# Optimization experiments

Measured on AMD Instinct MI355X. Metric: run time of the kernel, lower is better.

## Reference

```python
import jax, jax.numpy as jnp
import numpy as np

B, S, D = 2, 2048, 2048
NH, HD = 32, 64          # query heads, head_dim
NKV, NREP = 8, 4         # kv heads, num_key_value_groups
ROPE_THETA = 10000.0


def _rope_cos_sin(seq_len, head_dim, dtype=jnp.float32):
    inv_freq = 1.0 / (ROPE_THETA ** (jnp.arange(0, head_dim, 2, dtype=jnp.float32) / head_dim))
    pos = jnp.arange(seq_len, dtype=jnp.float32)
    freqs = jnp.outer(pos, inv_freq)               # [S, HD/2]
    emb = jnp.concatenate([freqs, freqs], axis=-1)  # [S, HD]
    return jnp.cos(emb).astype(dtype), jnp.sin(emb).astype(dtype)


def _rotate_half(x):
    x1, x2 = jnp.split(x, 2, axis=-1)
    return jnp.concatenate([-x2, x1], axis=-1)


def setup_inputs() -> dict:
    key = jax.random.key(0)
    k1, k2, k3, k4, k5 = jax.random.split(key, 5)
    scale = 0.02
    hidden_states = jax.random.normal(k1, (B, S, D), dtype=jnp.float32)
    Wq = jax.random.normal(k2, (NH * HD, D), dtype=jnp.float32) * scale
    Wk = jax.random.normal(k3, (NKV * HD, D), dtype=jnp.float32) * scale
    Wv = jax.random.normal(k4, (NKV * HD, D), dtype=jnp.float32) * scale
    Wo = jax.random.normal(k5, (D, NH * HD), dtype=jnp.float32) * scale
    # additive causal mask [B, 1, S, S]: 0 on/below diagonal, large negative above
    causal = jnp.triu(jnp.full((S, S), -1e9, dtype=jnp.float32), k=1)
    attention_mask = jnp.broadcast_to(causal[None, None], (B, 1, S, S))
    return {"hidden_states": hidden_states, "Wq": Wq, "Wk": Wk, "Wv": Wv,
            "Wo": Wo, "attention_mask": attention_mask}


def reference(hidden_states, Wq, Wk, Wv, Wo, attention_mask):
    bsz, q_len, _ = hidden_states.shape
    # projections (torch Linear: x @ W^T)
    q = (hidden_states @ Wq.T).reshape(bsz, q_len, NH, HD).transpose(0, 2, 1, 3)   # [B,NH,S,HD]
    k = (hidden_states @ Wk.T).reshape(bsz, q_len, NKV, HD).transpose(0, 2, 1, 3)  # [B,NKV,S,HD]
    v = (hidden_states @ Wv.T).reshape(bsz, q_len, NKV, HD).transpose(0, 2, 1, 3)
    # RoPE
    cos, sin = _rope_cos_sin(q_len, HD, hidden_states.dtype)  # [S,HD]
    cos = cos[None, None]  # [1,1,S,HD] (unsqueeze_dim=1 over broadcast batch)
    sin = sin[None, None]
    q = q * cos + _rotate_half(q) * sin
    k = k * cos + _rotate_half(k) * sin
    # repeat_kv (GQA): [B,NKV,S,HD] -> [B,NH,S,HD]
    k = jnp.repeat(k, NREP, axis=1)
    v = jnp.repeat(v, NREP, axis=1)
    # eager attention with materialized scores (faithful to the source)
    scores = jnp.einsum('bhqd,bhkd->bhqk', q, k) / jnp.sqrt(jnp.float32(HD))
    scores = scores + attention_mask[:, :, :, :q_len]
    probs = jax.nn.softmax(scores.astype(jnp.float32), axis=-1).astype(q.dtype)
    out = jnp.einsum('bhqk,bhkd->bhqd', probs, v)          # [B,NH,S,HD]
    out = out.transpose(0, 2, 1, 3).reshape(bsz, q_len, NH * HD)
    return out @ Wo.T
```

## Files before the change

kernel.cpp:

```cpp
#include <hip/hip_runtime.h>


#define S_LEN 2048
#define D_MODEL 2048
#define NHEAD 32
#define HEAD_DIM 64
#define NKVH 8
#define M_ROWS 4096
#define KVW (NKVH * HEAD_DIM)

typedef __attribute__((ext_vector_type(4))) float f32x4;
typedef __attribute__((ext_vector_type(8))) short bf16x8;

#define MFMA16(a, b, c) __builtin_amdgcn_mfma_f32_16x16x32_bf16((a), (b), (c), 0, 0, 0)

#define GLOAD_LDS16(g, l)                                                     \
    __builtin_amdgcn_global_load_lds(                                         \
        (const __attribute__((address_space(1))) void*)(g),                   \
        (__attribute__((address_space(3))) void*)(l), 16, 0, 0)

static __device__ __forceinline__ unsigned short f2bf(float f) {
    union { __bf16 b; unsigned short u; } v;
    v.b = (__bf16)f;
    return v.u;
}

static __device__ __forceinline__ float fexp2(float x) {
#if __has_builtin(__builtin_amdgcn_exp2f)
    return __builtin_amdgcn_exp2f(x);
#else
    return exp2f(x);
#endif
}

static __device__ __forceinline__ void xcd_swz(int& bx, int& by) {
    const int gx = gridDim.x;
    const int nwg = gx * gridDim.y;
    int lin = blockIdx.y * gx + blockIdx.x;
    lin = (lin & 7) * (nwg >> 3) + (lin >> 3);
    bx = lin % gx;
    by = lin / gx;
}

static __device__ bool detect_f32_block(const unsigned short* __restrict__ h) {
    __shared__ int dcnt;
    if (threadIdx.x == 0) dcnt = 0;
    __syncthreads();
    const unsigned short v = h[2 * (threadIdx.x & 255)];
    const int e = (v >> 7) & 0xFF;
    if (threadIdx.x < 256 && e >= 0x8D) atomicAdd(&dcnt, 1);
    __syncthreads();
    return dcnt >= 8;
}

static __device__ __forceinline__ bf16x8 load_frag(bool f32p, const void* p, size_t off) {
    if (f32p) {
        const float* fp = (const float*)p + off;
        f32x4 x = *reinterpret_cast<const f32x4*>(fp);
        f32x4 y = *reinterpret_cast<const f32x4*>(fp + 4);
        bf16x8 r;
        r[0] = (short)f2bf(x[0]); r[1] = (short)f2bf(x[1]);
        r[2] = (short)f2bf(x[2]); r[3] = (short)f2bf(x[3]);
        r[4] = (short)f2bf(y[0]); r[5] = (short)f2bf(y[1]);
        r[6] = (short)f2bf(y[2]); r[7] = (short)f2bf(y[3]);
        return r;
    }
    return *reinterpret_cast<const bf16x8*>((const unsigned short*)p + off);
}

__global__ __launch_bounds__(256) void cvt_all(const void* __restrict__ h,
                                               const void* __restrict__ wq,
                                               const void* __restrict__ wk,
                                               const void* __restrict__ wv,
                                               const void* __restrict__ wo,
                                               unsigned short* __restrict__ hbuf,
                                               unsigned short* __restrict__ wqb,
                                               unsigned short* __restrict__ wkvb,
                                               unsigned short* __restrict__ wob,
                                               float2* __restrict__ ropetab) {
    const bool f32p = detect_f32_block((const unsigned short*)h);
    const int e0 = 1048576;
    const int e1 = e0 + 524288;
    const int e2 = e1 + 131072;
    const int e3 = e2 + 131072;
    const int e4 = e3 + 524288;
    const int e5 = e4 + 8192;
    int i = blockIdx.x * 256 + threadIdx.x;
    const int stride = gridDim.x * 256;
    for (; i < e5; i += stride) {
        if (i >= e4) {
            const int base = (i - e4) * 8;
#pragma unroll
            for (int j = 0; j < 8; ++j) {
                const int idx = base + j;
                const int s = idx >> 5, dd = idx & 31;
                const float inv = exp2f(-(float)dd * 0.4152410118609203f);
                const float th = (float)s * inv;
                float sn, cs;
                sincosf(th, &sn, &cs);
                ropetab[idx] = make_float2(cs, sn);
            }
            continue;
        }
        const void* s;
        unsigned short* d;
        size_t off;
        if (i < e0)      { s = h;  d = hbuf; off = (size_t)i; }
        else if (i < e1) { s = wq; d = wqb;  off = (size_t)(i - e0); }
        else if (i < e2) { s = wk; d = wkvb; off = (size_t)(i - e1); }
        else if (i < e3) { s = wv; d = wkvb + (size_t)512 * 2048; off = (size_t)(i - e2); }
        else             { s = wo; d = wob;  off = (size_t)(i - e3); }
        bf16x8 v = load_frag(f32p, s, off * 8);
        *reinterpret_cast<bf16x8*>(d + off * 8) = v;
    }
}

static __device__ __forceinline__ void rope4_tab(const float2* __restrict__ tab,
                                                 const float (&vals)[4], float (&outv)[4],
                                                 int m, int l16) {
    const int s = m & (S_LEN - 1);
#pragma unroll
    for (int nt = 0; nt < 4; ++nt) {
        const int d = nt * 16 + l16;
        const float2 cs = tab[s * 32 + (d & 31)];
        const float part = vals[nt ^ 2];
        const float rot = (nt < 2) ? -part : part;
        outv[nt] = vals[nt] * cs.x + rot * cs.y;
    }
}

static __device__ __forceinline__ void rope4(const float (&vals)[4], float (&outv)[4],
                                             int m, int l16) {
    const float sf = (float)(m & (S_LEN - 1));
#pragma unroll
    for (int nt = 0; nt < 4; ++nt) {
        const int d = nt * 16 + l16;
        const float inv = exp2f(-(float)(d & 31) * 0.4152410118609203f);
        const float th = sf * inv;
        float sn, cs;
        sincosf(th, &sn, &cs);
        const float part = vals[nt ^ 2];
        const float rot = (nt < 2) ? -part : part;
        outv[nt] = vals[nt] * cs + rot * sn;
    }
}

__global__ __launch_bounds__(256) void gemm_qkv_lds(const unsigned short* __restrict__ A,
                                                    const unsigned short* __restrict__ W,
                                                    unsigned short* __restrict__ Qo,
                                                    unsigned short* __restrict__ KVo,
                                                    const float2* __restrict__ ropetab) {
    __shared__ unsigned short lds_a[128 * 32];
    __shared__ unsigned short lds_b[128 * 32];

    const int wave = threadIdx.x >> 6;
    const int lane = threadIdx.x & 63;
    const int l16  = lane & 15;
    const int quad = lane >> 4;
    const int wm   = wave >> 1;
    const int wn   = wave & 1;

    int bx, by;
    xcd_swz(bx, by);
    const int m0 = bx * 128;
    const int n0 = by * 128;

    const int srow = lane >> 2;
    const int scol = (lane & 3) * 8;
    const unsigned short* ag[2];
    const unsigned short* wg[2];
#pragma unroll
    for (int i = 0; i < 2; ++i) {
        const int c = wave * 2 + i;
        ag[i] = A + (size_t)(m0 + c * 16 + srow) * D_MODEL + scol;
        wg[i] = W + (size_t)(n0 + c * 16 + srow) * D_MODEL + scol;
    }

    f32x4 acc[4][4];
#pragma unroll
    for (int i = 0; i < 4; ++i)
#pragma unroll
        for (int j = 0; j < 4; ++j) acc[i][j] = (f32x4){0.f, 0.f, 0.f, 0.f};

    for (int k0 = 0; k0 < D_MODEL; k0 += 32) {
#pragma unroll
        for (int i = 0; i < 2; ++i) {
            const int c = wave * 2 + i;
            GLOAD_LDS16(ag[i] + k0, &lds_a[c * 512]);
            GLOAD_LDS16(wg[i] + k0, &lds_b[c * 512]);
        }
        __syncthreads();

        bf16x8 af[4], bfm[4];
#pragma unroll
        for (int t = 0; t < 4; ++t) {
            af[t]  = *reinterpret_cast<const bf16x8*>(&lds_a[(wm * 64 + t * 16 + l16) * 32 + quad * 8]);
            bfm[t] = *reinterpret_cast<const bf16x8*>(&lds_b[(wn * 64 + t * 16 + l16) * 32 + quad * 8]);
        }
#pragma unroll
        for (int mt = 0; mt < 4; ++mt)
#pragma unroll
            for (int nt = 0; nt < 4; ++nt)
                acc[mt][nt] = MFMA16(af[mt], bfm[nt], acc[mt][nt]);
        __syncthreads();
    }

    const int ncol0 = n0 + wn * 64;
    const bool do_rope = (ncol0 < 2048 + KVW);
    unsigned short* dst;
    int cstride, c0;
    if (ncol0 < 2048) { dst = Qo;  cstride = 2048; c0 = ncol0; }
    else              { dst = KVo; cstride = 1024; c0 = ncol0 - 2048; }

#pragma unroll
    for (int mt = 0; mt < 4; ++mt) {
#pragma unroll
        for (int r = 0; r < 4; ++r) {
            const int m = m0 + wm * 64 + mt * 16 + quad * 4 + r;
            float vals[4];
#pragma unroll
            for (int nt = 0; nt < 4; ++nt) vals[nt] = acc[mt][nt][r];
            float outv[4];
            if (do_rope) {
                rope4_tab(ropetab, vals, outv, m, l16);
            } else {
#pragma unroll
                for (int nt = 0; nt < 4; ++nt) outv[nt] = vals[nt];
            }
            unsigned short* cp = dst + (size_t)m * cstride + c0;
#pragma unroll
            for (int nt = 0; nt < 4; ++nt) cp[nt * 16 + l16] = f2bf(outv[nt]);
        }
    }
}

__global__ __launch_bounds__(256) void gemm_bt_lds(const unsigned short* __restrict__ A,
                                                   const unsigned short* __restrict__ W,
                                                   void* __restrict__ Cp, int N,
                                                   const unsigned short* __restrict__ hdet,
                                                   int rope, int finalout) {
    __shared__ unsigned short lds_a[128 * 32];
    __shared__ unsigned short lds_b[128 * 32];

    bool of32 = false;
    if (finalout) of32 = detect_f32_block(hdet);

    const int wave = threadIdx.x >> 6;
    const int lane = threadIdx.x & 63;
    const int l16  = lane & 15;
    const int quad = lane >> 4;
    const int wm   = wave >> 1;
    const int wn   = wave & 1;

    int bx, by;
    xcd_swz(bx, by);
    const int m0 = bx * 128;
    const int n0 = by * 128;

    const int srow = lane >> 2;
    const int scol = (lane & 3) * 8;
    const unsigned short* ag[2];
    const unsigned short* wg[2];
#pragma unroll
    for (int i = 0; i < 2; ++i) {
        const int c = wave * 2 + i;
        ag[i] = A + (size_t)(m0 + c * 16 + srow) * D_MODEL + scol;
        wg[i] = W + (size_t)(n0 + c * 16 + srow) * D_MODEL + scol;
    }

    f32x4 acc[4][4];
#pragma unroll
    for (int i = 0; i < 4; ++i)
#pragma unroll
        for (int j = 0; j < 4; ++j) acc[i][j] = (f32x4){0.f, 0.f, 0.f, 0.f};

    for (int k0 = 0; k0 < D_MODEL; k0 += 32) {
#pragma unroll
        for (int i = 0; i < 2; ++i) {
            const int c = wave * 2 + i;
            GLOAD_LDS16(ag[i] + k0, &lds_a[c * 512]);
            GLOAD_LDS16(wg[i] + k0, &lds_b[c * 512]);
        }
        __syncthreads();

        bf16x8 af[4], bfm[4];
#pragma unroll
        for (int t = 0; t < 4; ++t) {
            af[t]  = *reinterpret_cast<const bf16x8*>(&lds_a[(wm * 64 + t * 16 + l16) * 32 + quad * 8]);
            bfm[t] = *reinterpret_cast<const bf16x8*>(&lds_b[(wn * 64 + t * 16 + l16) * 32 + quad * 8]);
        }
#pragma unroll
        for (int mt = 0; mt < 4; ++mt)
#pragma unroll
            for (int nt = 0; nt < 4; ++nt)
                acc[mt][nt] = MFMA16(af[mt], bfm[nt], acc[mt][nt]);
        __syncthreads();
    }

    const bool do_rope = (rope != 0);
    const int ncol0 = n0 + wn * 64;

#pragma unroll
    for (int mt = 0; mt < 4; ++mt) {
#pragma unroll
        for (int r = 0; r < 4; ++r) {
            const int m = m0 + wm * 64 + mt * 16 + quad * 4 + r;
            float vals[4];
#pragma unroll
            for (int nt = 0; nt < 4; ++nt) vals[nt] = acc[mt][nt][r];
            float outv[4];
            if (do_rope) {
                rope4(vals, outv, m, l16);
            } else {
#pragma unroll
                for (int nt = 0; nt < 4; ++nt) outv[nt] = vals[nt];
            }
            const size_t crow = (size_t)m * N + ncol0;
            if (of32) {
                float* cp = (float*)Cp + crow;
#pragma unroll
                for (int nt = 0; nt < 4; ++nt) cp[nt * 16 + l16] = outv[nt];
            } else {
                unsigned short* cp = (unsigned short*)Cp + crow;
#pragma unroll
                for (int nt = 0; nt < 4; ++nt) cp[nt * 16 + l16] = f2bf(outv[nt]);
            }
        }
    }
}

__global__ __launch_bounds__(256) void transpose_v(const unsigned short* __restrict__ Vsrc,
                                                   unsigned short* __restrict__ Vt) {
    __shared__ unsigned short t[64][72];
    const int bid = blockIdx.x;
    const int ct = bid & 7;
    const int st = (bid >> 3) & 31;
    const int b  = bid >> 8;
    const unsigned short* src = Vsrc + ((size_t)b * S_LEN + st * 64) * 1024 + ct * 64;
    unsigned short* dst = Vt + ((size_t)b * KVW + ct * 64) * S_LEN + st * 64;
    const int r0 = threadIdx.x >> 3;
    const int c0 = (threadIdx.x & 7) * 8;
#pragma unroll
    for (int h = 0; h < 2; ++h) {
        bf16x8 v = *reinterpret_cast<const bf16x8*>(src + (size_t)(r0 + h * 32) * 1024 + c0);
        *reinterpret_cast<bf16x8*>(&t[r0 + h * 32][c0]) = v;
    }
    __syncthreads();
#pragma unroll
    for (int h = 0; h < 2; ++h) {
        const int cr = r0 + h * 32;
        bf16x8 v;
#pragma unroll
        for (int j = 0; j < 8; ++j) v[j] = (short)t[c0 + j][cr];
        *reinterpret_cast<bf16x8*>(dst + (size_t)cr * S_LEN + c0) = v;
    }
}

struct AttnCtx {
    const unsigned short* qbase;
    const unsigned short* kbase;
    const unsigned short* vtbase;
    unsigned short* obase;
    int kvs;
    int l16, quad;
    unsigned short (*lpw)[72];
};

#define SM_C 0.18033688011112042f
#define SM_THR 8.0f

static __device__ __forceinline__ void attn_qtile(const AttnCtx& cx, int q0w) {
    const int l16 = cx.l16, quad = cx.quad;
    const int kvs = cx.kvs;

    bf16x8 ones;
#pragma unroll
    for (int j = 0; j < 8; ++j) ones[j] = (short)0x3F80;

    bf16x8 aq[2][2];
#pragma unroll
    for (int m = 0; m < 2; ++m)
#pragma unroll
        for (int kh = 0; kh < 2; ++kh)
            aq[m][kh] = *reinterpret_cast<const bf16x8*>(
                cx.qbase + (size_t)(q0w + m * 16 + l16) * D_MODEL + kh * 32 + quad * 8);

    f32x4 o[2][4];
    f32x4 c_l[2];
#pragma unroll
    for (int m = 0; m < 2; ++m) {
#pragma unroll
        for (int i = 0; i < 4; ++i) o[m][i] = (f32x4){0.f, 0.f, 0.f, 0.f};
        c_l[m] = (f32x4){0.f, 0.f, 0.f, 0.f};
    }
    float m2[2][4];
#pragma unroll
    for (int m = 0; m < 2; ++m)
#pragma unroll
        for (int r = 0; r < 4; ++r) m2[m][r] = 0.f;

    const int kv_hi = q0w + 32;

    for (int k0 = 0; k0 < kv_hi; k0 += 64) {
        bf16x8 kf[8];
#pragma unroll
        for (int t = 0; t < 4; ++t) {
            const unsigned short* krow = cx.kbase + (size_t)(k0 + t * 16 + l16) * kvs;
            kf[2 * t]     = *reinterpret_cast<const bf16x8*>(krow + quad * 8);
            kf[2 * t + 1] = *reinterpret_cast<const bf16x8*>(krow + 32 + quad * 8);
        }

        f32x4 sc[2][4];
        __builtin_amdgcn_s_setprio(1);
#pragma unroll
        for (int t = 0; t < 4; ++t) {
#pragma unroll
            for (int m = 0; m < 2; ++m) {
                f32x4 c = (f32x4){0.f, 0.f, 0.f, 0.f};
                c = MFMA16(aq[m][0], kf[2 * t], c);
                c = MFMA16(aq[m][1], kf[2 * t + 1], c);
                sc[m][t] = c;
            }
        }
        __builtin_amdgcn_s_setprio(0);

        bf16x8 vf[8];
#pragma unroll
        for (int nt = 0; nt < 4; ++nt) {
            const unsigned short* vrow =
                cx.vtbase + (size_t)(nt * 16 + l16) * S_LEN + k0 + quad * 8;
            vf[2 * nt]     = *reinterpret_cast<const bf16x8*>(vrow);
            vf[2 * nt + 1] = *reinterpret_cast<const bf16x8*>(vrow + 32);
        }

        const bool full = (k0 + 63 <= q0w);
        float pm[2][4];
        float dif = -3.0e38f;
#pragma unroll
        for (int m = 0; m < 2; ++m) {
#pragma unroll
            for (int r = 0; r < 4; ++r) {
                const int qi = q0w + m * 16 + quad * 4 + r;
                float s[4];
#pragma unroll
                for (int t = 0; t < 4; ++t) {
                    s[t] = sc[m][t][r] * SM_C;
                    if (!full && (k0 + t * 16 + l16 > qi)) s[t] = -1.0e30f;
                    sc[m][t][r] = s[t];
                }
                const float p = fmaxf(fmaxf(s[0], s[1]), fmaxf(s[2], s[3]));
                pm[m][r] = p;
                dif = fmaxf(dif, p - m2[m][r]);
            }
        }
        if (__any(dif > SM_THR)) {
#pragma unroll
            for (int m = 0; m < 2; ++m) {
#pragma unroll
                for (int r = 0; r < 4; ++r) {
                    float mt = pm[m][r];
#pragma unroll
                    for (int off = 1; off < 16; off <<= 1)
                        mt = fmaxf(mt, __shfl_xor(mt, off, 64));
                    const float mn = fmaxf(m2[m][r], mt);
                    const float al = fexp2(m2[m][r] - mn);
                    m2[m][r] = mn;
#pragma unroll
                    for (int nt = 0; nt < 4; ++nt) o[m][nt][r] *= al;
                    c_l[m][r] *= al;
                }
            }
        }
#pragma unroll
        for (int m = 0; m < 2; ++m) {
#pragma unroll
            for (int r = 0; r < 4; ++r) {
                const float mb = m2[m][r];
#pragma unroll
                for (int t = 0; t < 4; ++t) {
                    const float pv = fexp2(sc[m][t][r] - mb);
                    cx.lpw[m * 16 + quad * 4 + r][t * 16 + l16] = f2bf(pv);
                }
            }
        }
        asm volatile("" ::: "memory");
        bf16x8 ap[2][2];
#pragma unroll
        for (int m = 0; m < 2; ++m)
#pragma unroll
            for (int kh = 0; kh < 2; ++kh)
                ap[m][kh] = *reinterpret_cast<const bf16x8*>(
                    &cx.lpw[m * 16 + l16][kh * 32 + quad * 8]);
        __builtin_amdgcn_s_setprio(1);
#pragma unroll
        for (int nt = 0; nt < 4; ++nt)
#pragma unroll
            for (int m = 0; m < 2; ++m) {
                o[m][nt] = MFMA16(ap[m][0], vf[2 * nt], o[m][nt]);
                o[m][nt] = MFMA16(ap[m][1], vf[2 * nt + 1], o[m][nt]);
            }
#pragma unroll
        for (int m = 0; m < 2; ++m) {
            c_l[m] = MFMA16(ap[m][0], ones, c_l[m]);
            c_l[m] = MFMA16(ap[m][1], ones, c_l[m]);
        }
        __builtin_amdgcn_s_setprio(0);
    }

#pragma unroll
    for (int m = 0; m < 2; ++m)
#pragma unroll
        for (int r = 0; r < 4; ++r) {
            const float inv_l = 1.0f / c_l[m][r];
            unsigned short* orow = cx.obase + (size_t)(q0w + m * 16 + quad * 4 + r) * D_MODEL;
#pragma unroll
            for (int nt = 0; nt < 4; ++nt)
                orow[nt * 16 + l16] = f2bf(o[m][nt][r] * inv_l);
        }
}

__global__ __launch_bounds__(256) void attn_kernel7(const unsigned short* __restrict__ Q,
                                                    const unsigned short* __restrict__ Kb,
                                                    const unsigned short* __restrict__ Vt,
                                                    unsigned short* __restrict__ O, int kvs) {
    __shared__ unsigned short lp[4][32][72];

    const int wave = threadIdx.x >> 6;
    const int lane = threadIdx.x & 63;

    const int bid  = blockIdx.x;
    const int qt   = 15 - (bid >> 6);
    const int bh   = bid & 63;
    const int h    = bh & (NHEAD - 1);
    const int b    = bh >> 5;
    const int kvh  = h >> 2;

    AttnCtx cx;
    cx.qbase  = Q + (size_t)b * S_LEN * D_MODEL + h * HEAD_DIM;
    cx.kbase  = Kb + (size_t)b * S_LEN * kvs + kvh * HEAD_DIM;
    cx.vtbase = Vt + ((size_t)b * KVW + kvh * HEAD_DIM) * S_LEN;
    cx.obase  = O + (size_t)b * S_LEN * D_MODEL + h * HEAD_DIM;
    cx.kvs    = kvs;
    cx.l16    = lane & 15;
    cx.quad   = lane >> 4;
    cx.lpw    = lp[wave];

    attn_qtile(cx, qt * 128 + wave * 32);
}

__global__ __launch_bounds__(256) void gemm_bt(const void* __restrict__ Ap,
                                               const void* __restrict__ Wp,
                                               void* __restrict__ Cp, int N,
                                               const unsigned short* __restrict__ hdet,
                                               int a_input, int rope, int finalout) {
    const bool isf32 = detect_f32_block(hdet);
    const bool af32 = isf32 && (a_input != 0);
    const bool wf32 = isf32;
    const bool of32 = isf32 && (finalout != 0);

    const int wave = threadIdx.x >> 6;
    const int lane = threadIdx.x & 63;
    const int l16  = lane & 15;
    const int quad = lane >> 4;
    const int m0 = blockIdx.x * 64 + wave * 16;
    const int n0 = blockIdx.y * 64;

    f32x4 acc[4];
#pragma unroll
    for (int i = 0; i < 4; ++i) acc[i] = (f32x4){0.f, 0.f, 0.f, 0.f};

    const size_t aoff = (size_t)(m0 + l16) * D_MODEL + quad * 8;
    size_t woff[4];
#pragma unroll
    for (int nt = 0; nt < 4; ++nt)
        woff[nt] = (size_t)(n0 + nt * 16 + l16) * D_MODEL + quad * 8;

    for (int k0 = 0; k0 < D_MODEL; k0 += 32) {
        bf16x8 a = load_frag(af32, Ap, aoff + k0);
#pragma unroll
        for (int nt = 0; nt < 4; ++nt) {
            bf16x8 b = load_frag(wf32, Wp, woff[nt] + k0);
            acc[nt] = MFMA16(a, b, acc[nt]);
        }
    }

#pragma unroll
    for (int r = 0; r < 4; ++r) {
        const int m = m0 + quad * 4 + r;
        float vals[4];
#pragma unroll
        for (int nt = 0; nt < 4; ++nt) vals[nt] = acc[nt][r];
        float outv[4];
        if (rope) {
            rope4(vals, outv, m, l16);
        } else {
#pragma unroll
            for (int nt = 0; nt < 4; ++nt) outv[nt] = vals[nt];
        }
        const size_t crow = (size_t)m * N + n0;
        if (of32) {
            float* cp = (float*)Cp + crow;
#pragma unroll
            for (int nt = 0; nt < 4; ++nt) cp[nt * 16 + l16] = outv[nt];
        } else {
            unsigned short* cp = (unsigned short*)Cp + crow;
#pragma unroll
            for (int nt = 0; nt < 4; ++nt) cp[nt * 16 + l16] = f2bf(outv[nt]);
        }
    }
}

__global__ __launch_bounds__(256) void attn_kernel(const unsigned short* __restrict__ Q,
                                                   const unsigned short* __restrict__ Kb,
                                                   const unsigned short* __restrict__ Vb,
                                                   unsigned short* __restrict__ O, int kvs) {
    __shared__ unsigned short lp[4][16][32];

    const int wave = threadIdx.x >> 6;
    const int lane = threadIdx.x & 63;
    const int l16  = lane & 15;
    const int quad = lane >> 4;

    const int bid = blockIdx.x;
    const int qb  = bid & 31;
    const int h   = (bid >> 5) & 31;
    const int b   = bid >> 10;
    const int kvh = h >> 2;
    const int q0  = qb * 64 + wave * 16;

    const unsigned short* qbase = Q + (size_t)b * S_LEN * D_MODEL + h * HEAD_DIM;
    const unsigned short* kbase = Kb + (size_t)b * S_LEN * kvs + kvh * HEAD_DIM;
    const unsigned short* vbase = Vb + (size_t)b * S_LEN * kvs + kvh * HEAD_DIM;

    bf16x8 aq0 = *reinterpret_cast<const bf16x8*>(qbase + (size_t)(q0 + l16) * D_MODEL + quad * 8);
    bf16x8 aq1 = *reinterpret_cast<const bf16x8*>(qbase + (size_t)(q0 + l16) * D_MODEL + 32 + quad * 8);

    f32x4 o[4];
#pragma unroll
    for (int i = 0; i < 4; ++i) o[i] = (f32x4){0.f, 0.f, 0.f, 0.f};
    float mrow[4], lrow[4];
#pragma unroll
    for (int r = 0; r < 4; ++r) { mrow[r] = -3.0e38f; lrow[r] = 0.f; }

    const int kv_hi = qb * 64 + 64;
    for (int k0 = 0; k0 < kv_hi; k0 += 32) {
        f32x4 sc[2];
#pragma unroll
        for (int t = 0; t < 2; ++t) {
            const unsigned short* krow = kbase + (size_t)(k0 + t * 16 + l16) * kvs;
            bf16x8 b0 = *reinterpret_cast<const bf16x8*>(krow + quad * 8);
            bf16x8 b1 = *reinterpret_cast<const bf16x8*>(krow + 32 + quad * 8);
            f32x4 c = (f32x4){0.f, 0.f, 0.f, 0.f};
            c = MFMA16(aq0, b0, c);
            c = MFMA16(aq1, b1, c);
            sc[t] = c;
        }

        float alpha[4], p0v[4], p1v[4];
#pragma unroll
        for (int r = 0; r < 4; ++r) {
            const int qi = q0 + quad * 4 + r;
            float s0 = sc[0][r] * 0.125f;
            float s1 = sc[1][r] * 0.125f;
            if (k0 + l16 > qi)       s0 = -1.0e30f;
            if (k0 + 16 + l16 > qi)  s1 = -1.0e30f;
            float mt = fmaxf(s0, s1);
#pragma unroll
            for (int off = 1; off < 16; off <<= 1) mt = fmaxf(mt, __shfl_xor(mt, off, 64));
            const float mn = fmaxf(mrow[r], mt);
            const float al = __expf(mrow[r] - mn);
            const float p0 = __expf(s0 - mn);
            const float p1 = __expf(s1 - mn);
            float rs = p0 + p1;
#pragma unroll
            for (int off = 1; off < 16; off <<= 1) rs += __shfl_xor(rs, off, 64);
            lrow[r] = lrow[r] * al + rs;
            mrow[r] = mn;
            alpha[r] = al;
            p0v[r] = p0; p1v[r] = p1;
        }
#pragma unroll
        for (int nt = 0; nt < 4; ++nt)
#pragma unroll
            for (int r = 0; r < 4; ++r) o[nt][r] *= alpha[r];

        __syncthreads();
#pragma unroll
        for (int r = 0; r < 4; ++r) {
            lp[wave][quad * 4 + r][l16]      = f2bf(p0v[r]);
            lp[wave][quad * 4 + r][16 + l16] = f2bf(p1v[r]);
        }
        __syncthreads();
        bf16x8 ap = *reinterpret_cast<const bf16x8*>(&lp[wave][l16][quad * 8]);

#pragma unroll
        for (int nt = 0; nt < 4; ++nt) {
            const unsigned short* vcol = vbase + nt * 16 + l16 + (size_t)(k0 + quad * 8) * kvs;
            bf16x8 bv;
#pragma unroll
            for (int j = 0; j < 8; ++j) bv[j] = (short)vcol[(size_t)j * kvs];
            o[nt] = MFMA16(ap, bv, o[nt]);
        }
    }

    unsigned short* obase = O + (size_t)b * S_LEN * D_MODEL + h * HEAD_DIM;
#pragma unroll
    for (int r = 0; r < 4; ++r) {
        const float inv_l = 1.0f / lrow[r];
        unsigned short* orow = obase + (size_t)(q0 + quad * 4 + r) * D_MODEL;
#pragma unroll
        for (int nt = 0; nt < 4; ++nt)
            orow[nt * 16 + l16] = f2bf(o[nt][r] * inv_l);
    }
}

extern "C" void kernel_launch(void* const* d_in, const int* in_sizes, int n_in,
                              void* d_out, int out_size, void* d_ws, size_t ws_size,
                              hipStream_t stream) {
    const void* hidden = d_in[0];
    const void* Wq = d_in[1];
    const void* Wk = d_in[2];
    const void* Wv = d_in[3];
    const void* Wo = d_in[4];

    char* ws = (char*)d_ws;
    dim3 blk(256);

    const size_t NEED = 1024 + ((size_t)64 << 20) + (512u << 10);
    if (ws_size >= NEED) {
        unsigned short* kvbuf = (unsigned short*)(ws + 1024);
        unsigned short* abuf  = kvbuf + (size_t)4096 * 1024;
        unsigned short* hbuf  = abuf + (size_t)4096 * 2048;
        unsigned short* wqb   = hbuf + (size_t)4096 * 2048;
        unsigned short* wkvb  = wqb + (size_t)2048 * 2048;
        unsigned short* wob   = wkvb + (size_t)1024 * 2048;
        unsigned short* vtbuf = wob + (size_t)2048 * 2048;
        float2* ropetab       = (float2*)(vtbuf + (size_t)2 * 512 * 2048);
        unsigned short* qbuf  = (unsigned short*)d_out;

        cvt_all<<<dim3(2048), blk, 0, stream>>>(hidden, Wq, Wk, Wv, Wo,
                                                hbuf, wqb, wkvb, wob, ropetab);

        gemm_qkv_lds<<<dim3(32, 24), blk, 0, stream>>>(hbuf, wqb, qbuf, kvbuf, ropetab);
        transpose_v<<<dim3(512), blk, 0, stream>>>(kvbuf + 512, vtbuf);
        attn_kernel7<<<dim3(2 * NHEAD * (S_LEN / 128)), blk, 0, stream>>>(qbuf, kvbuf, vtbuf, abuf, 1024);
        gemm_bt_lds<<<dim3(32, 16), blk, 0, stream>>>(abuf, wob, d_out, 2048,
                                                      (const unsigned short*)hidden, 0, 1);
    } else {
        unsigned short* kbuf = (unsigned short*)(ws + 1024);
        unsigned short* vbuf = (unsigned short*)(ws + 1024 + (4u << 20));
        unsigned short* abuf = (unsigned short*)(ws + 1024 + (8u << 20));
        unsigned short* qbuf = (unsigned short*)d_out;
        const unsigned short* hdet = (const unsigned short*)hidden;
        gemm_bt<<<dim3(M_ROWS / 64, D_MODEL / 64), blk, 0, stream>>>(hidden, Wq, qbuf, D_MODEL, hdet, 1, 1, 0);
        gemm_bt<<<dim3(M_ROWS / 64, (NKVH * HEAD_DIM) / 64), blk, 0, stream>>>(hidden, Wk, kbuf, NKVH * HEAD_DIM, hdet, 1, 1, 0);
        gemm_bt<<<dim3(M_ROWS / 64, (NKVH * HEAD_DIM) / 64), blk, 0, stream>>>(hidden, Wv, vbuf, NKVH * HEAD_DIM, hdet, 1, 0, 0);
        attn_kernel<<<dim3(2 * NHEAD * (S_LEN / 64)), blk, 0, stream>>>(qbuf, kbuf, vbuf, abuf, 512);
        gemm_bt<<<dim3(M_ROWS / 64, D_MODEL / 64), blk, 0, stream>>>(abuf, Wo, d_out, D_MODEL, hdet, 0, 0, 1);
    }
}
```

Before: 426.2 us.

## Double-buffer LDS tiles in QKV and output GEMM main loops

Both the QKV-projection and the generic bf16 GEMM kernels now keep two LDS stages for the A and W tiles. Each iteration issues the async global-to-LDS loads for the next K slice before running the MFMAs on the current slice, and one barrier per iteration replaces the previous two. The aim is to hide global load latency behind matrix-core work, at the cost of doubling the LDS footprint per block, which may lower occupancy.

```diff
diff --git a/kernel.cpp b/kernel.cpp
--- a/kernel.cpp
+++ b/kernel.cpp
@@ -145,13 +145,48 @@
     }
 }
 
+#define GEMM_STAGE(BB, KK)                                                    \
+    {                                                                         \
+        _Pragma("unroll")                                                     \
+        for (int i_ = 0; i_ < 2; ++i_) {                                      \
+            const int c_ = wave * 2 + i_;                                     \
+            GLOAD_LDS16(ag[i_] + (KK), &lds_a[BB][c_ * 512]);                 \
+            GLOAD_LDS16(wg[i_] + (KK), &lds_b[BB][c_ * 512]);                 \
+        }                                                                     \
+    }
+
+#define GEMM_MAINLOOP()                                                       \
+    GEMM_STAGE(0, 0);                                                         \
+    __syncthreads();                                                          \
+    {                                                                         \
+        int cur = 0;                                                          \
+        for (int k0 = 0; k0 < D_MODEL; k0 += 32) {                            \
+            if (k0 + 32 < D_MODEL) GEMM_STAGE(cur ^ 1, k0 + 32);              \
+            bf16x8 af[4], bfm[4];                                             \
+            _Pragma("unroll")                                                 \
+            for (int t = 0; t < 4; ++t) {                                     \
+                af[t]  = *reinterpret_cast<const bf16x8*>(                    \
+                    &lds_a[cur][(wm * 64 + t * 16 + l16) * 32 + quad * 8]);   \
+                bfm[t] = *reinterpret_cast<const bf16x8*>(                    \
+                    &lds_b[cur][(wn * 64 + t * 16 + l16) * 32 + quad * 8]);   \
+            }                                                                 \
+            _Pragma("unroll")                                                 \
+            for (int mt = 0; mt < 4; ++mt)                                    \
+                _Pragma("unroll")                                             \
+                for (int nt = 0; nt < 4; ++nt)                                \
+                    acc[mt][nt] = MFMA16(af[mt], bfm[nt], acc[mt][nt]);       \
+            __syncthreads();                                                  \
+            cur ^= 1;                                                         \
+        }                                                                     \
+    }
+
 __global__ __launch_bounds__(256) void gemm_qkv_lds(const unsigned short* __restrict__ A,
                                                     const unsigned short* __restrict__ W,
                                                     unsigned short* __restrict__ Qo,
                                                     unsigned short* __restrict__ KVo,
                                                     const float2* __restrict__ ropetab) {
-    __shared__ unsigned short lds_a[128 * 32];
-    __shared__ unsigned short lds_b[128 * 32];
+    __shared__ unsigned short lds_a[2][128 * 32];
+    __shared__ unsigned short lds_b[2][128 * 32];
 
     const int wave = threadIdx.x >> 6;
     const int lane = threadIdx.x & 63;
@@ -182,28 +217,7 @@
 #pragma unroll
         for (int j = 0; j < 4; ++j) acc[i][j] = (f32x4){0.f, 0.f, 0.f, 0.f};
 
-    for (int k0 = 0; k0 < D_MODEL; k0 += 32) {
-#pragma unroll
-        for (int i = 0; i < 2; ++i) {
-            const int c = wave * 2 + i;
-            GLOAD_LDS16(ag[i] + k0, &lds_a[c * 512]);
-            GLOAD_LDS16(wg[i] + k0, &lds_b[c * 512]);
-        }
-        __syncthreads();
-
-        bf16x8 af[4], bfm[4];
-#pragma unroll
-        for (int t = 0; t < 4; ++t) {
-            af[t]  = *reinterpret_cast<const bf16x8*>(&lds_a[(wm * 64 + t * 16 + l16) * 32 + quad * 8]);
-            bfm[t] = *reinterpret_cast<const bf16x8*>(&lds_b[(wn * 64 + t * 16 + l16) * 32 + quad * 8]);
-        }
-#pragma unroll
-        for (int mt = 0; mt < 4; ++mt)
-#pragma unroll
-            for (int nt = 0; nt < 4; ++nt)
-                acc[mt][nt] = MFMA16(af[mt], bfm[nt], acc[mt][nt]);
-        __syncthreads();
-    }
+    GEMM_MAINLOOP();
 
     const int ncol0 = n0 + wn * 64;
     const bool do_rope = (ncol0 < 2048 + KVW);
@@ -239,8 +253,8 @@
                                                    void* __restrict__ Cp, int N,
                                                    const unsigned short* __restrict__ hdet,
                                                    int rope, int finalout) {
-    __shared__ unsigned short lds_a[128 * 32];
-    __shared__ unsigned short lds_b[128 * 32];
+    __shared__ unsigned short lds_a[2][128 * 32];
+    __shared__ unsigned short lds_b[2][128 * 32];
 
     bool of32 = false;
     if (finalout) of32 = detect_f32_block(hdet);
@@ -274,28 +288,7 @@
 #pragma unroll
         for (int j = 0; j < 4; ++j) acc[i][j] = (f32x4){0.f, 0.f, 0.f, 0.f};
 
-    for (int k0 = 0; k0 < D_MODEL; k0 += 32) {
-#pragma unroll
-        for (int i = 0; i < 2; ++i) {
-            const int c = wave * 2 + i;
-            GLOAD_LDS16(ag[i] + k0, &lds_a[c * 512]);
-            GLOAD_LDS16(wg[i] + k0, &lds_b[c * 512]);
-        }
-        __syncthreads();
-
-        bf16x8 af[4], bfm[4];
-#pragma unroll
-        for (int t = 0; t < 4; ++t) {
-            af[t]  = *reinterpret_cast<const bf16x8*>(&lds_a[(wm * 64 + t * 16 + l16) * 32 + quad * 8]);
-            bfm[t] = *reinterpret_cast<const bf16x8*>(&lds_b[(wn * 64 + t * 16 + l16) * 32 + quad * 8]);
-        }
-#pragma unroll
-        for (int mt = 0; mt < 4; ++mt)
-#pragma unroll
-            for (int nt = 0; nt < 4; ++nt)
-                acc[mt][nt] = MFMA16(af[mt], bfm[nt], acc[mt][nt]);
-        __syncthreads();
-    }
+    GEMM_MAINLOOP();
 
     const bool do_rope = (rope != 0);
     const int ncol0 = n0 + wn * 64;
```

New measurement: 423.8 us. Within noise of the previous version (-0.6%).
